# Optimization experiments

Hardware: AMD Instinct MI355X
Metric: run time of the kernel (lower is better)

The kernel has to match this reference:

```python
import jax, jax.numpy as jnp
import numpy as np

NH = 4        # router attention heads
M1, M2 = 16, 16  # Fourier modes kept
N_FNO_LAYERS = 4
TOP_K = 2
TEMP = 1.0


def _ln(x, g, b):
    m = x.mean(-1, keepdims=True)
    v = ((x - m) ** 2).mean(-1, keepdims=True)
    return (x - m) / jnp.sqrt(v + 1e-5) * g + b


def _mha(s, wqkv, bqkv, wo, bo):
    B, S, D = s.shape
    dh = D // NH
    qkv = s @ wqkv + bqkv
    q, k, v = jnp.split(qkv, 3, axis=-1)
    rs = lambda t: t.reshape(B, S, NH, dh).transpose(0, 2, 1, 3)
    q, k, v = rs(q), rs(k), rs(v)
    a = jax.nn.softmax(jnp.einsum('bhqd,bhkd->bhqk', q, k) / np.sqrt(dh), axis=-1)
    o = jnp.einsum('bhqk,bhkd->bhqd', a, v).transpose(0, 2, 1, 3).reshape(B, S, D)
    return o @ wo + bo


def _spectral_conv(h, w1, w2):
    # h: (B, Ci, H, W); w1/w2: (Ci, Co, M1, M2, 2) real/imag pairs
    B, Ci, H, W = h.shape
    Co = w1.shape[1]
    ft = jnp.fft.rfft2(h, axes=(-2, -1))  # (B, Ci, H, W//2+1) complex
    w1c = w1[..., 0] + 1j * w1[..., 1]
    w2c = w2[..., 0] + 1j * w2[..., 1]
    lo = jnp.einsum('bixy,ioxy->boxy', ft[:, :, :M1, :M2], w1c)
    hi = jnp.einsum('bixy,ioxy->boxy', ft[:, :, -M1:, :M2], w2c)
    oft = jnp.zeros((B, Co, H, W // 2 + 1), dtype=ft.dtype)
    oft = oft.at[:, :, :M1, :M2].set(lo).at[:, :, -M1:, :M2].set(hi)
    return jnp.fft.irfft2(oft, s=(H, W), axes=(-2, -1))


def _fno(x, lw, lb, sw1, sw2, kw, kb, p1w, p1b, p2w, p2b):
    h = jnp.einsum('bchw,co->bohw', x, lw) + lb[None, :, None, None]
    for l in range(N_FNO_LAYERS):
        s = _spectral_conv(h, sw1[l], sw2[l])
        sk = jnp.einsum('bchw,co->bohw', h, kw[l]) + kb[l][None, :, None, None]
        h = s + sk
        if l < N_FNO_LAYERS - 1:
            h = jax.nn.gelu(h)
    h = jax.nn.gelu(jnp.einsum('bchw,co->bohw', h, p1w) + p1b[None, :, None, None])
    return jnp.einsum('bchw,co->bohw', h, p2w) + p2b[None, :, None, None]


def _router(x, enc_in_w, enc_in_b, attn_wqkv, attn_bqkv, attn_wo, attn_bo,
            ln1_g, ln1_b, ffn_w1, ffn_b1, ffn_w2, ffn_b2, ln2_g, ln2_b, fc_w, fc_b):
    ic = x[:, :, 0, :]                       # (B, C, W) initial condition
    s = ic.transpose(0, 2, 1) @ enc_in_w + enc_in_b  # (B, W, hd)
    for l in range(attn_wqkv.shape[0]):
        s = _ln(s + _mha(s, attn_wqkv[l], attn_bqkv[l], attn_wo[l], attn_bo[l]), ln1_g[l], ln1_b[l])
        f = jax.nn.relu(s @ ffn_w1[l] + ffn_b1[l]) @ ffn_w2[l] + ffn_b2[l]
        s = _ln(s + f, ln2_g[l], ln2_b[l])
    feat = s.max(axis=1)                     # global max-pool over sequence
    logits = feat @ fc_w + fc_b              # (B, E)
    vals, idx = jax.lax.top_k(logits, TOP_K)
    w = jax.nn.softmax(vals / TEMP, axis=-1)
    B = logits.shape[0]
    rw = jnp.zeros_like(logits).at[jnp.arange(B)[:, None], idx].set(w)
    return rw


def setup_inputs() -> dict:
    key = jax.random.key(0)
    ks = iter(jax.random.split(key, 40))
    B, C, H, W = 32, 1, 64, 64
    E, HC, HD, RL, FF, OC = 8, 64, 64, 2, 256, 1
    rn = lambda shp, sc: jax.random.normal(next(ks), shp, dtype=jnp.float32) * sc
    inp = {
        'x': rn((B, C, H, W), 1.0),
        'enc_in_w': rn((C, HD), 0.5), 'enc_in_b': jnp.zeros((HD,), jnp.float32),
        'attn_wqkv': rn((RL, HD, 3 * HD), 0.08), 'attn_bqkv': jnp.zeros((RL, 3 * HD), jnp.float32),
        'attn_wo': rn((RL, HD, HD), 0.08), 'attn_bo': jnp.zeros((RL, HD), jnp.float32),
        'ln1_g': jnp.ones((RL, HD), jnp.float32), 'ln1_b': jnp.zeros((RL, HD), jnp.float32),
        'ffn_w1': rn((RL, HD, FF), 0.08), 'ffn_b1': jnp.zeros((RL, FF), jnp.float32),
        'ffn_w2': rn((RL, FF, HD), 0.05), 'ffn_b2': jnp.zeros((RL, HD), jnp.float32),
        'ln2_g': jnp.ones((RL, HD), jnp.float32), 'ln2_b': jnp.zeros((RL, HD), jnp.float32),
        'fc_w': rn((HD, E), 0.1), 'fc_b': jnp.zeros((E,), jnp.float32),
        'lift_w': rn((E, C, HC), 0.3), 'lift_b': jnp.zeros((E, HC), jnp.float32),
        'spec_w1': rn((E, N_FNO_LAYERS, HC, HC, M1, M2, 2), 1.0 / HC),
        'spec_w2': rn((E, N_FNO_LAYERS, HC, HC, M1, M2, 2), 1.0 / HC),
        'skip_w': rn((E, N_FNO_LAYERS, HC, HC), 0.08), 'skip_b': jnp.zeros((E, N_FNO_LAYERS, HC), jnp.float32),
        'proj1_w': rn((E, HC, HC), 0.08), 'proj1_b': jnp.zeros((E, HC), jnp.float32),
        'proj2_w': rn((E, HC, OC), 0.08), 'proj2_b': jnp.zeros((E, OC), jnp.float32),
    }
    return inp


def reference(x, enc_in_w, enc_in_b, attn_wqkv, attn_bqkv, attn_wo, attn_bo,
              ln1_g, ln1_b, ffn_w1, ffn_b1, ffn_w2, ffn_b2, ln2_g, ln2_b, fc_w, fc_b,
              lift_w, lift_b, spec_w1, spec_w2, skip_w, skip_b,
              proj1_w, proj1_b, proj2_w, proj2_b):
    rw = _router(x, enc_in_w, enc_in_b, attn_wqkv, attn_bqkv, attn_wo, attn_bo,
                 ln1_g, ln1_b, ffn_w1, ffn_b1, ffn_w2, ffn_b2, ln2_g, ln2_b, fc_w, fc_b)
    E = rw.shape[1]
    out = jnp.zeros((x.shape[0], proj2_w.shape[2], x.shape[2], x.shape[3]), x.dtype)
    for e in range(E):
        # weight is 0 for non-selected experts, so dense weighted sum == masked dispatch
        y = _fno(x, lift_w[e], lift_b[e], spec_w1[e], spec_w2[e],
                 skip_w[e], skip_b[e], proj1_w[e], proj1_b[e], proj2_w[e], proj2_b[e])
        out = out + rw[:, e, None, None, None] * y
    return out
```

## Files before the change

### kernel.cpp

```cpp
#include <hip/hip_runtime.h>
#include <math.h>

#define TWOPI_F 6.283185307179586f
#define LD4(p) (*(const float4*)(p))

__device__ __forceinline__ float gelu_f(float v) {
    float u = 0.7978845608028654f * (v + 0.044715f * v * v * v);
    return 0.5f * v * (1.f + tanhf(u));
}

__global__ void init_tables_kernel(float* __restrict__ Wy, float* __restrict__ TWX,
                                   float* __restrict__ WY2) {
    int t = threadIdx.x;
    for (int i = t; i < 1024; i += 256) {
        int y = i >> 4, k = i & 15;
        int m = (k * y) & 63;
        float a = -TWOPI_F * (float)m / 64.f;
        Wy[y * 32 + 2 * k]     = cosf(a);
        Wy[y * 32 + 2 * k + 1] = sinf(a);
    }
    for (int i = t; i < 2048; i += 256) {
        int x = i >> 5, kxm = i & 31;
        int kx = kxm < 16 ? kxm : kxm + 32;
        int m = (kx * x) & 63;
        float a = -TWOPI_F * (float)m / 64.f;
        TWX[x * 64 + 2 * kxm]     = cosf(a);
        TWX[x * 64 + 2 * kxm + 1] = sinf(a);
    }
    for (int i = t; i < 1024; i += 256) {
        int y = i >> 4, k = i & 15;
        int m = (k * y) & 63;
        float a = TWOPI_F * (float)m / 64.f;
        float sc = (k == 0 ? 1.f : 2.f) / 4096.f;
        WY2[y * 32 + 2 * k]     = sc * cosf(a);
        WY2[y * 32 + 2 * k + 1] = sc * sinf(a);
    }
}

__global__ __launch_bounds__(512) void router_kernel(
    const float* __restrict__ x, const float* __restrict__ enc_w, const float* __restrict__ enc_b,
    const float* __restrict__ wqkv, const float* __restrict__ bqkv,
    const float* __restrict__ wo, const float* __restrict__ bo,
    const float* __restrict__ ln1g, const float* __restrict__ ln1b,
    const float* __restrict__ w1, const float* __restrict__ b1,
    const float* __restrict__ w2, const float* __restrict__ b2,
    const float* __restrict__ ln2g, const float* __restrict__ ln2b,
    const float* __restrict__ fcw, const float* __restrict__ fcb,
    float* __restrict__ rw)
{
    __shared__ float s[64][65];
    __shared__ float qk[64][193];
    __shared__ float sc[64][65];
    __shared__ float o64[64][65];
    __shared__ float feat[64];
    __shared__ float logits[8];
    int b = blockIdx.x, t = threadIdx.x;

    for (int i = t; i < 4096; i += 512) {
        int w_ = i >> 6, d = i & 63;
        s[w_][d] = x[b * 4096 + w_] * enc_w[d] + enc_b[d];
    }
    __syncthreads();

    for (int l = 0; l < 2; ++l) {
        {
            const float* Wq = wqkv + l * 64 * 192;
            const float* Bq = bqkv + l * 192;
            int c4 = t % 48, rg = t / 48;
            if (rg < 8) {
                const float* wcol = Wq + 4 * c4;
                float4 bq = LD4(Bq + 4 * c4);
                float4 acc[8];
#pragma unroll
                for (int i = 0; i < 8; ++i) acc[i] = bq;
                int r0 = rg * 8;
#pragma unroll 8
                for (int k = 0; k < 64; ++k) {
                    float4 wv = LD4(wcol + k * 192);
#pragma unroll
                    for (int i = 0; i < 8; ++i) {
                        float sv = s[r0 + i][k];
                        acc[i].x += sv * wv.x; acc[i].y += sv * wv.y;
                        acc[i].z += sv * wv.z; acc[i].w += sv * wv.w;
                    }
                }
#pragma unroll
                for (int i = 0; i < 8; ++i) {
                    qk[r0 + i][4 * c4]     = acc[i].x;
                    qk[r0 + i][4 * c4 + 1] = acc[i].y;
                    qk[r0 + i][4 * c4 + 2] = acc[i].z;
                    qk[r0 + i][4 * c4 + 3] = acc[i].w;
                }
            }
        }
        __syncthreads();
        for (int h = 0; h < 4; ++h) {
            for (int i = t; i < 4096; i += 512) {
                int q = i >> 6, kj = i & 63;
                float acc = 0.f;
#pragma unroll
                for (int d = 0; d < 16; ++d)
                    acc += qk[q][h * 16 + d] * qk[kj][64 + h * 16 + d];
                sc[q][kj] = acc * 0.25f;
            }
            __syncthreads();
            if (t < 64) {
                float m = -1e30f;
                for (int j = 0; j < 64; ++j) m = fmaxf(m, sc[t][j]);
                float sum = 0.f;
                for (int j = 0; j < 64; ++j) { float e2 = expf(sc[t][j] - m); sc[t][j] = e2; sum += e2; }
                float inv = 1.f / sum;
                for (int j = 0; j < 64; ++j) sc[t][j] *= inv;
            }
            __syncthreads();
            for (int i = t; i < 1024; i += 512) {
                int q = i >> 4, d = i & 15;
                float acc = 0.f;
#pragma unroll 8
                for (int j = 0; j < 64; ++j) acc += sc[q][j] * qk[j][128 + h * 16 + d];
                o64[q][h * 16 + d] = acc;
            }
            __syncthreads();
        }
        {
            const float* Wo = wo + l * 4096;
            const float* Bo = bo + l * 64;
            int c4 = t & 15, rg = t >> 4;
            const float* wcol = Wo + 4 * c4;
            float4 acc0 = LD4(Bo + 4 * c4), acc1 = acc0;
            int r0 = rg * 2;
#pragma unroll 8
            for (int k = 0; k < 64; ++k) {
                float4 wv = LD4(wcol + k * 64);
                float h0 = o64[r0][k], h1 = o64[r0 + 1][k];
                acc0.x += h0 * wv.x; acc0.y += h0 * wv.y;
                acc0.z += h0 * wv.z; acc0.w += h0 * wv.w;
                acc1.x += h1 * wv.x; acc1.y += h1 * wv.y;
                acc1.z += h1 * wv.z; acc1.w += h1 * wv.w;
            }
            sc[r0][4 * c4]     = s[r0][4 * c4]     + acc0.x;
            sc[r0][4 * c4 + 1] = s[r0][4 * c4 + 1] + acc0.y;
            sc[r0][4 * c4 + 2] = s[r0][4 * c4 + 2] + acc0.z;
            sc[r0][4 * c4 + 3] = s[r0][4 * c4 + 3] + acc0.w;
            sc[r0 + 1][4 * c4]     = s[r0 + 1][4 * c4]     + acc1.x;
            sc[r0 + 1][4 * c4 + 1] = s[r0 + 1][4 * c4 + 1] + acc1.y;
            sc[r0 + 1][4 * c4 + 2] = s[r0 + 1][4 * c4 + 2] + acc1.z;
            sc[r0 + 1][4 * c4 + 3] = s[r0 + 1][4 * c4 + 3] + acc1.w;
        }
        __syncthreads();
        if (t < 64) {
            float m = 0.f;
            for (int j = 0; j < 64; ++j) m += sc[t][j];
            m *= (1.f / 64.f);
            float v = 0.f;
            for (int j = 0; j < 64; ++j) { float d = sc[t][j] - m; v += d * d; }
            v *= (1.f / 64.f);
            float inv = rsqrtf(v + 1e-5f);
            for (int j = 0; j < 64; ++j)
                s[t][j] = (sc[t][j] - m) * inv * ln1g[l * 64 + j] + ln1b[l * 64 + j];
        }
        __syncthreads();
        {
            const float* W1 = w1 + l * 64 * 256;
            const float* B1 = b1 + l * 256;
            int c4 = t & 63, rg = t >> 6;
            const float* wcol = W1 + 4 * c4;
            float4 b1v = LD4(B1 + 4 * c4);
            float4 acc[8];
#pragma unroll
            for (int i = 0; i < 8; ++i) acc[i] = b1v;
            int r0 = rg * 8;
#pragma unroll 4
            for (int k = 0; k < 64; ++k) {
                float4 wv = LD4(wcol + k * 256);
#pragma unroll
                for (int i = 0; i < 8; ++i) {
                    float sv = s[r0 + i][k];
                    acc[i].x += sv * wv.x; acc[i].y += sv * wv.y;
                    acc[i].z += sv * wv.z; acc[i].w += sv * wv.w;
                }
            }
#pragma unroll
            for (int i = 0; i < 8; ++i) {
                float a0 = fmaxf(acc[i].x, 0.f), a1 = fmaxf(acc[i].y, 0.f);
                float a2 = fmaxf(acc[i].z, 0.f), a3 = fmaxf(acc[i].w, 0.f);
                if (c4 < 48) {
                    qk[r0 + i][4 * c4] = a0; qk[r0 + i][4 * c4 + 1] = a1;
                    qk[r0 + i][4 * c4 + 2] = a2; qk[r0 + i][4 * c4 + 3] = a3;
                } else {
                    int c = 4 * c4 - 192;
                    o64[r0 + i][c] = a0; o64[r0 + i][c + 1] = a1;
                    o64[r0 + i][c + 2] = a2; o64[r0 + i][c + 3] = a3;
                }
            }
        }
        __syncthreads();
        {
            const float* W2 = w2 + l * 256 * 64;
            const float* B2 = b2 + l * 64;
            int c4 = t & 15, rg = t >> 4;
            const float* wcol = W2 + 4 * c4;
            float4 acc0 = LD4(B2 + 4 * c4), acc1 = acc0;
            int r0 = rg * 2;
#pragma unroll 8
            for (int k = 0; k < 192; ++k) {
                float4 wv = LD4(wcol + k * 64);
                float h0 = qk[r0][k], h1 = qk[r0 + 1][k];
                acc0.x += h0 * wv.x; acc0.y += h0 * wv.y;
                acc0.z += h0 * wv.z; acc0.w += h0 * wv.w;
                acc1.x += h1 * wv.x; acc1.y += h1 * wv.y;
                acc1.z += h1 * wv.z; acc1.w += h1 * wv.w;
            }
#pragma unroll 8
            for (int k = 192; k < 256; ++k) {
                float4 wv = LD4(wcol + k * 64);
                float h0 = o64[r0][k - 192], h1 = o64[r0 + 1][k - 192];
                acc0.x += h0 * wv.x; acc0.y += h0 * wv.y;
                acc0.z += h0 * wv.z; acc0.w += h0 * wv.w;
                acc1.x += h1 * wv.x; acc1.y += h1 * wv.y;
                acc1.z += h1 * wv.z; acc1.w += h1 * wv.w;
            }
            sc[r0][4 * c4]     = s[r0][4 * c4]     + acc0.x;
            sc[r0][4 * c4 + 1] = s[r0][4 * c4 + 1] + acc0.y;
            sc[r0][4 * c4 + 2] = s[r0][4 * c4 + 2] + acc0.z;
            sc[r0][4 * c4 + 3] = s[r0][4 * c4 + 3] + acc0.w;
            sc[r0 + 1][4 * c4]     = s[r0 + 1][4 * c4]     + acc1.x;
            sc[r0 + 1][4 * c4 + 1] = s[r0 + 1][4 * c4 + 1] + acc1.y;
            sc[r0 + 1][4 * c4 + 2] = s[r0 + 1][4 * c4 + 2] + acc1.z;
            sc[r0 + 1][4 * c4 + 3] = s[r0 + 1][4 * c4 + 3] + acc1.w;
        }
        __syncthreads();
        if (t < 64) {
            float m = 0.f;
            for (int j = 0; j < 64; ++j) m += sc[t][j];
            m *= (1.f / 64.f);
            float v = 0.f;
            for (int j = 0; j < 64; ++j) { float d = sc[t][j] - m; v += d * d; }
            v *= (1.f / 64.f);
            float inv = rsqrtf(v + 1e-5f);
            for (int j = 0; j < 64; ++j)
                s[t][j] = (sc[t][j] - m) * inv * ln2g[l * 64 + j] + ln2b[l * 64 + j];
        }
        __syncthreads();
    }
    if (t < 64) {
        float m = -1e30f;
        for (int r = 0; r < 64; ++r) m = fmaxf(m, s[r][t]);
        feat[t] = m;
    }
    __syncthreads();
    if (t < 8) {
        float acc = fcb[t];
        for (int k = 0; k < 64; ++k) acc += feat[k] * fcw[k * 8 + t];
        logits[t] = acc;
    }
    __syncthreads();
    if (t == 0) {
        int i0 = 0;
        for (int j = 1; j < 8; ++j) if (logits[j] > logits[i0]) i0 = j;
        int i1 = -1;
        for (int j = 0; j < 8; ++j) {
            if (j == i0) continue;
            if (i1 < 0 || logits[j] > logits[i1]) i1 = j;
        }
        float e1 = expf(logits[i1] - logits[i0]);
        float w0 = 1.f / (1.f + e1);
        float w1v = e1 / (1.f + e1);
        for (int j = 0; j < 8; ++j) rw[b * 8 + j] = 0.f;
        rw[b * 8 + i0] = w0;
        rw[b * 8 + i1] = w1v;
    }
}

__global__ void build_pairs_kernel(const float* __restrict__ rw, int* __restrict__ pair_b,
                                   int* __restrict__ pair_e, float* __restrict__ pair_w,
                                   int* __restrict__ estart, int* __restrict__ chunk_e,
                                   int* __restrict__ chunk_p0, int* __restrict__ chunk_np) {
    __shared__ float r[256];
    __shared__ int cnt[8], off[9];
    int t = threadIdx.x;
    for (int i = t; i < 256; i += 64) r[i] = rw[i];
    if (t < 64) { pair_b[t] = 0; pair_e[t] = 0; pair_w[t] = 0.f; }
    __syncthreads();
    if (t < 8) {
        int c = 0;
        for (int b = 0; b < 32; ++b) if (r[b * 8 + t] != 0.f) ++c;
        cnt[t] = c;
    }
    __syncthreads();
    if (t == 0) {
        int a = 0;
        for (int e = 0; e < 8; ++e) { off[e] = a; a += cnt[e]; }
        off[8] = a;
        for (int e = 0; e <= 8; ++e) estart[e] = off[e];
        int nc = 0;
        for (int e = 0; e < 8; ++e) {
            for (int s = off[e]; s < off[e + 1]; s += 8) {
                int np = off[e + 1] - s; if (np > 8) np = 8;
                chunk_e[nc] = e; chunk_p0[nc] = s; chunk_np[nc] = np; ++nc;
            }
        }
        for (int c = nc; c < 16; ++c) { chunk_e[c] = 0; chunk_p0[c] = 0; chunk_np[c] = 0; }
    }
    __syncthreads();
    if (t < 8) {
        int n = off[t];
        for (int b = 0; b < 32; ++b) {
            float w = r[b * 8 + t];
            if (w != 0.f) { pair_b[n] = b; pair_e[n] = t; pair_w[n] = w; ++n; }
        }
    }
}

__global__ __launch_bounds__(256) void lift_kernel(const float* __restrict__ x,
    const float* __restrict__ lw, const float* __restrict__ lb,
    const int* __restrict__ pair_b, const int* __restrict__ pair_e, float* __restrict__ hA) {
    int p = blockIdx.x, tile = blockIdx.y, t = threadIdx.x;
    int b = pair_b[p], e = pair_e[p];
    float* h = hA + (size_t)p * 262144;
    const float* xb = x + (size_t)b * 4096;
    for (int i = tile * 16384 + t; i < (tile + 1) * 16384; i += 256) {
        int co = i >> 12, xy = i & 4095;
        h[i] = xb[xy] * lw[e * 64 + co] + lb[e * 64 + co];
    }
}

__global__ __launch_bounds__(256) void fwdft_kernel(const float* __restrict__ h,
    const float* __restrict__ Wy, float* __restrict__ F) {
    __shared__ float ht[64][68];
    __shared__ float gt[64][36];
    __shared__ float wy[2048];
    __shared__ float tw64[128];
    int bid = blockIdx.x;
    int t = threadIdx.x;
    const float* src = h + (size_t)bid * 4096;
    for (int i = t; i < 1024; i += 256) {
        float4 v = *(const float4*)(src + i * 4);
        int x = (i * 4) >> 6, y = (i * 4) & 63;
        *(float4*)(&ht[x][y]) = v;
    }
    for (int i = t; i < 512; i += 256) *(float4*)(&wy[i * 4]) = *(const float4*)(Wy + i * 4);
    if (t < 64) {
        float a = -TWOPI_F * (float)t / 64.f;
        tw64[2 * t]     = cosf(a);
        tw64[2 * t + 1] = sinf(a);
    }
    __syncthreads();
    {
        int xx = t >> 2, kq = t & 3;
        float gr0 = 0.f, gi0 = 0.f, gr1 = 0.f, gi1 = 0.f;
        float gr2 = 0.f, gi2 = 0.f, gr3 = 0.f, gi3 = 0.f;
#pragma unroll 4
        for (int y = 0; y < 64; ++y) {
            float hv = ht[xx][y];
            float4 w0 = *(const float4*)(&wy[y * 32 + kq * 8]);
            float4 w1 = *(const float4*)(&wy[y * 32 + kq * 8 + 4]);
            gr0 += hv * w0.x; gi0 += hv * w0.y;
            gr1 += hv * w0.z; gi1 += hv * w0.w;
            gr2 += hv * w1.x; gi2 += hv * w1.y;
            gr3 += hv * w1.z; gi3 += hv * w1.w;
        }
        *(float4*)(&gt[xx][kq * 8])     = make_float4(gr0, gi0, gr1, gi1);
        *(float4*)(&gt[xx][kq * 8 + 4]) = make_float4(gr2, gi2, gr3, gi3);
    }
    __syncthreads();
    {
        int kxm = t & 31, kyq = t >> 5;
        int kx = kxm < 16 ? kxm : kxm + 32;
        float ar0 = 0.f, ai0 = 0.f, ar1 = 0.f, ai1 = 0.f;
        int idx = 0;
#pragma unroll 4
        for (int xx = 0; xx < 64; ++xx) {
            float c_ = tw64[2 * idx], s_ = tw64[2 * idx + 1];
            float4 g = *(const float4*)(&gt[xx][kyq * 4]);
            ar0 += g.x * c_ - g.y * s_;  ai0 += g.x * s_ + g.y * c_;
            ar1 += g.z * c_ - g.w * s_;  ai1 += g.z * s_ + g.w * c_;
            idx = (idx + kx) & 63;
        }
        float* fb = F + (size_t)bid * 1024 + kxm * 32 + kyq * 4;
        *(float4*)(fb) = make_float4(ar0, ai0, ar1, ai1);
    }
}

__global__ __launch_bounds__(256) void spectral_kernel(
    const float* __restrict__ F, float* __restrict__ FoA, float* __restrict__ FoB,
    const float* __restrict__ w1, const float* __restrict__ w2,
    const int* __restrict__ chunk_e, const int* __restrict__ chunk_p0,
    const int* __restrict__ chunk_np, int l)
{
    int c = blockIdx.x;
    int np = chunk_np[c];
    if (np == 0) return;
    int e = chunk_e[c], p0 = chunk_p0[c];
    int z = blockIdx.z;
    int wsel = z & 1, cih = (z >> 1) & 1, mq = z >> 2;
    int t = threadIdx.x;
    int co = blockIdx.y * 4 + (t >> 6);
    int lane = t & 63;
    int moff = mq * 256 + lane * 4;

    const float* wbase = (wsel == 0 ? w1 : w2) + (size_t)(e * 4 + l) * 2097152;
    const float* Wc  = wbase + (size_t)(cih * 32) * 32768 + (size_t)co * 512 + moff;
    const float* Fc0 = F + (size_t)p0 * 65536 + (size_t)(cih * 32) * 1024 + wsel * 512 + moff;
    float* Fob = (cih ? FoB : FoA) + (size_t)p0 * 65536 + (size_t)co * 1024 + wsel * 512 + moff;

    float4 acc[8];
#pragma unroll
    for (int p = 0; p < 8; ++p) acc[p] = make_float4(0.f, 0.f, 0.f, 0.f);
    const float* Wp = Wc;
    const float* Fp = Fc0;
    for (int ci = 0; ci < 32; ++ci) {
        float4 wv = LD4(Wp);
#pragma unroll
        for (int p = 0; p < 8; ++p) {
            float4 fv = LD4(Fp + (size_t)p * 65536);
            acc[p].x += fv.x * wv.x - fv.y * wv.y;
            acc[p].y += fv.x * wv.y + fv.y * wv.x;
            acc[p].z += fv.z * wv.z - fv.w * wv.w;
            acc[p].w += fv.z * wv.w + fv.w * wv.z;
        }
        Wp += 32768;
        Fp += 1024;
    }
#pragma unroll
    for (int p = 0; p < 8; ++p) {
        if (p < np)
            *(float4*)(Fob + (size_t)p * 65536) = acc[p];
    }
}

__global__ __launch_bounds__(256) void conv1x1_kernel(
    const float* __restrict__ src, float* __restrict__ dst,
    const float* __restrict__ Wall, const float* __restrict__ Ball,
    const int* __restrict__ pair_e, int wmul, int wadd, int do_gelu)
{
    __shared__ float ws[64][68];
    __shared__ float bs[64];
    int p = blockIdx.x, tile = blockIdx.y, t = threadIdx.x;
    int e = pair_e[p];
    int widx = e * wmul + wadd;
    const float* W = Wall + (size_t)widx * 4096;
    for (int i = t; i < 1024; i += 256) {
        float4 v = LD4(W + i * 4);
        int ci = (i * 4) >> 6, co = (i * 4) & 63;
        *(float4*)(&ws[ci][co]) = v;
    }
    if (t < 64) bs[t] = Ball[widx * 64 + t];
    __syncthreads();

    int xy4 = t & 63, cog = t >> 6;
    const float* sb = src + (size_t)p * 262144 + tile * 256 + xy4 * 4;
    float4 acc[16];
#pragma unroll
    for (int j = 0; j < 16; ++j) {
        float bv = bs[cog * 16 + j];
        acc[j] = make_float4(bv, bv, bv, bv);
    }
    for (int ci = 0; ci < 64; ++ci) {
        float4 sv = LD4(sb + (size_t)ci * 4096);
        float4 w0 = *(const float4*)(&ws[ci][cog * 16]);
        float4 w1 = *(const float4*)(&ws[ci][cog * 16 + 4]);
        float4 w2 = *(const float4*)(&ws[ci][cog * 16 + 8]);
        float4 w3 = *(const float4*)(&ws[ci][cog * 16 + 12]);
        float wr[16] = {w0.x, w0.y, w0.z, w0.w, w1.x, w1.y, w1.z, w1.w,
                        w2.x, w2.y, w2.z, w2.w, w3.x, w3.y, w3.z, w3.w};
#pragma unroll
        for (int j = 0; j < 16; ++j) {
            float w = wr[j];
            acc[j].x += sv.x * w; acc[j].y += sv.y * w;
            acc[j].z += sv.z * w; acc[j].w += sv.w * w;
        }
    }
    float* d = dst + (size_t)p * 262144 + (size_t)(cog * 16) * 4096 + tile * 256 + xy4 * 4;
#pragma unroll
    for (int j = 0; j < 16; ++j) {
        float4 v = acc[j];
        if (do_gelu) {
            v.x = gelu_f(v.x); v.y = gelu_f(v.y);
            v.z = gelu_f(v.z); v.w = gelu_f(v.w);
        }
        *(float4*)(d + (size_t)j * 4096) = v;
    }
}

__global__ __launch_bounds__(256) void inv_kernel(
    const float* __restrict__ FoA, const float* __restrict__ FoB,
    const float* __restrict__ WY2, float* __restrict__ dst_h, int do_gelu)
{
    __shared__ float wy2[2048];
    __shared__ float twl[128];
    __shared__ float fo_s[1024];
    __shared__ float tT[64][36];
    __shared__ float ot[64][66];
    int t = threadIdx.x;
    for (int i = t; i < 512; i += 256) *(float4*)(&wy2[i * 4]) = *(const float4*)(WY2 + i * 4);
    if (t < 64) {
        float a = TWOPI_F * (float)t / 64.f;
        twl[2 * t] = cosf(a);
        twl[2 * t + 1] = sinf(a);
    }
    __syncthreads();

    for (int item = 0; item < 4; ++item) {
        int wid = blockIdx.x * 4 + item;
        int p = wid >> 6, co = wid & 63;
        const float* fA = FoA + (size_t)p * 65536 + (size_t)co * 1024;
        const float* fB = FoB + (size_t)p * 65536 + (size_t)co * 1024;
        {
            float4 a = LD4(fA + t * 4);
            float4 b = LD4(fB + t * 4);
            *(float4*)(&fo_s[t * 4]) = make_float4(a.x + b.x, a.y + b.y, a.z + b.z, a.w + b.w);
        }
        __syncthreads();
        {
            int xx = t & 63, kq = t >> 6;
            float Tr0 = 0.f, Ti0 = 0.f, Tr1 = 0.f, Ti1 = 0.f;
            float Tr2 = 0.f, Ti2 = 0.f, Tr3 = 0.f, Ti3 = 0.f;
#pragma unroll 4
            for (int kxm = 0; kxm < 32; ++kxm) {
                int kx = kxm < 16 ? kxm : kxm + 32;
                int idx = (kx * xx) & 63;
                float c_ = twl[2 * idx], s_ = twl[2 * idx + 1];
                float4 f0 = *(const float4*)(&fo_s[kxm * 32 + kq * 8]);
                float4 f1 = *(const float4*)(&fo_s[kxm * 32 + kq * 8 + 4]);
                Tr0 += f0.x * c_ - f0.y * s_;  Ti0 += f0.x * s_ + f0.y * c_;
                Tr1 += f0.z * c_ - f0.w * s_;  Ti1 += f0.z * s_ + f0.w * c_;
                Tr2 += f1.x * c_ - f1.y * s_;  Ti2 += f1.x * s_ + f1.y * c_;
                Tr3 += f1.z * c_ - f1.w * s_;  Ti3 += f1.z * s_ + f1.w * c_;
            }
            *(float4*)(&tT[xx][kq * 8])     = make_float4(Tr0, Ti0, Tr1, Ti1);
            *(float4*)(&tT[xx][kq * 8 + 4]) = make_float4(Tr2, Ti2, Tr3, Ti3);
        }
        __syncthreads();
        {
            int xx = t & 63, yq = t >> 6;
            float Trr[16], Tii[16];
#pragma unroll
            for (int q = 0; q < 8; ++q) {
                float4 v = *(const float4*)(&tT[xx][q * 4]);
                Trr[q * 2] = v.x; Tii[q * 2] = v.y;
                Trr[q * 2 + 1] = v.z; Tii[q * 2 + 1] = v.w;
            }
            for (int j = 0; j < 16; ++j) {
                int y = yq * 16 + j;
                const float* wr = &wy2[y * 32];
                float acc = 0.f;
#pragma unroll
                for (int k = 0; k < 16; ++k)
                    acc += Trr[k] * wr[2 * k] - Tii[k] * wr[2 * k + 1];
                ot[xx][y] = acc;
            }
        }
        __syncthreads();
        {
            float* base = dst_h + (size_t)p * 262144 + (size_t)co * 4096;
            for (int r = 0; r < 16; ++r) {
                int gidx = r * 256 + t;
                int xx = gidx >> 6, y = gidx & 63;
                float v = base[gidx] + ot[xx][y];
                if (do_gelu) v = gelu_f(v);
                base[gidx] = v;
            }
        }
        __syncthreads();
    }
}

__global__ __launch_bounds__(256) void proj2_kernel(
    const float* __restrict__ hsrc, const float* __restrict__ p2w, const float* __restrict__ p2b,
    const int* __restrict__ pair_b, const int* __restrict__ pair_e,
    const float* __restrict__ pw, float* __restrict__ out)
{
    int p = blockIdx.x, tile = blockIdx.y, t = threadIdx.x;
    int b = pair_b[p], e = pair_e[p];
    float wgt = pw[p];
    const float* h = hsrc + (size_t)p * 262144 + tile * 256 + t;
    const float* w2 = p2w + e * 64;
    float acc = p2b[e];
#pragma unroll
    for (int c = 0; c < 64; ++c) acc += h[(size_t)c * 4096] * w2[c];
    atomicAdd(out + (size_t)b * 4096 + tile * 256 + t, wgt * acc);
}

extern "C" void kernel_launch(void* const* d_in, const int* in_sizes, int n_in,
                              void* d_out, int out_size, void* d_ws, size_t ws_size,
                              hipStream_t stream) {
    const float* x    = (const float*)d_in[0];
    const float* encw = (const float*)d_in[1];
    const float* encb = (const float*)d_in[2];
    const float* wqkv = (const float*)d_in[3];
    const float* bqkv = (const float*)d_in[4];
    const float* wo   = (const float*)d_in[5];
    const float* bo   = (const float*)d_in[6];
    const float* ln1g = (const float*)d_in[7];
    const float* ln1b = (const float*)d_in[8];
    const float* fw1  = (const float*)d_in[9];
    const float* fb1  = (const float*)d_in[10];
    const float* fw2  = (const float*)d_in[11];
    const float* fb2  = (const float*)d_in[12];
    const float* ln2g = (const float*)d_in[13];
    const float* ln2b = (const float*)d_in[14];
    const float* fcw  = (const float*)d_in[15];
    const float* fcb  = (const float*)d_in[16];
    const float* lw   = (const float*)d_in[17];
    const float* lb   = (const float*)d_in[18];
    const float* sw1  = (const float*)d_in[19];
    const float* sw2  = (const float*)d_in[20];
    const float* skw  = (const float*)d_in[21];
    const float* skb  = (const float*)d_in[22];
    const float* p1w  = (const float*)d_in[23];
    const float* p1b  = (const float*)d_in[24];
    const float* p2w  = (const float*)d_in[25];
    const float* p2b  = (const float*)d_in[26];
    float* out = (float*)d_out;

    float* wsf    = (float*)d_ws;
    float* rw     = wsf;
    float* pair_w = wsf + 256;
    int*   ipart  = (int*)(wsf + 320);
    int* pair_b   = ipart;
    int* pair_e   = ipart + 64;
    int* estart   = ipart + 128;
    int* chunk_e  = ipart + 137;
    int* chunk_p0 = ipart + 153;
    int* chunk_np = ipart + 169;
    float* Wy  = wsf + 512;
    float* TWX = wsf + 2560;
    float* WY2 = wsf + 6656;
    float* hA  = wsf + 16384;
    float* hB  = hA + (size_t)64 * 262144;
    float* F   = hB + (size_t)64 * 262144;
    float* FoA = F + (size_t)64 * 65536;
    float* FoB = FoA + (size_t)64 * 65536;
    size_t need = (16384 + 2ull * 64 * 262144 + 64ull * 65536 + 64ull * 131072) * 4;
    if (ws_size < need) return;

    hipMemsetAsync(d_out, 0, (size_t)out_size * sizeof(float), stream);
    init_tables_kernel<<<1, 256, 0, stream>>>(Wy, TWX, WY2);
    router_kernel<<<32, 512, 0, stream>>>(x, encw, encb, wqkv, bqkv, wo, bo, ln1g, ln1b,
                                          fw1, fb1, fw2, fb2, ln2g, ln2b, fcw, fcb, rw);
    build_pairs_kernel<<<1, 64, 0, stream>>>(rw, pair_b, pair_e, pair_w, estart,
                                             chunk_e, chunk_p0, chunk_np);
    lift_kernel<<<dim3(64, 16), 256, 0, stream>>>(x, lw, lb, pair_b, pair_e, hA);
    for (int l = 0; l < 4; ++l) {
        float* cur = (l & 1) ? hB : hA;
        float* nxt = (l & 1) ? hA : hB;
        fwdft_kernel<<<4096, 256, 0, stream>>>(cur, Wy, F);
        spectral_kernel<<<dim3(16, 16, 8), 256, 0, stream>>>(F, FoA, FoB, sw1, sw2,
                                                             chunk_e, chunk_p0, chunk_np, l);
        conv1x1_kernel<<<dim3(64, 16), 256, 0, stream>>>(cur, nxt, skw, skb, pair_e, 4, l, 0);
        inv_kernel<<<1024, 256, 0, stream>>>(FoA, FoB, WY2, nxt, (l < 3) ? 1 : 0);
    }
    conv1x1_kernel<<<dim3(64, 16), 256, 0, stream>>>(hA, hB, p1w, p1b, pair_e, 1, 0, 1);
    proj2_kernel<<<dim3(64, 16), 256, 0, stream>>>(hB, p2w, p2b, pair_b, pair_e, pair_w, out);
}
```

Baseline: 1.422 ms.

## Fuse projection layers, precompute twiddle tables, and split inverse DFT into more blocks

Merges the proj1 1x1 conv, GELU and the proj2 reduction into one kernel, so the full hidden tensor is no longer written to and re-read from global memory before the final projection. The per-block twiddle computation with cosf/sinf in the forward and inverse DFT kernels is replaced by a load of a small precomputed table. The inverse kernel now handles one (pair, channel) item per block across 4096 blocks instead of looping over 4 items per block, which gives more parallelism but repeats the WY2 table load per block.

Result: faster. 1.322 ms (-7.1%).

```diff
diff --git a/kernel.cpp b/kernel.cpp
--- a/kernel.cpp
+++ b/kernel.cpp
@@ -19,13 +19,12 @@
         Wy[y * 32 + 2 * k]     = cosf(a);
         Wy[y * 32 + 2 * k + 1] = sinf(a);
     }
-    for (int i = t; i < 2048; i += 256) {
-        int x = i >> 5, kxm = i & 31;
-        int kx = kxm < 16 ? kxm : kxm + 32;
-        int m = (kx * x) & 63;
-        float a = -TWOPI_F * (float)m / 64.f;
-        TWX[x * 64 + 2 * kxm]     = cosf(a);
-        TWX[x * 64 + 2 * kxm + 1] = sinf(a);
+    if (t < 64) {
+        float a = -TWOPI_F * (float)t / 64.f;
+        TWX[2 * t]           = cosf(a);
+        TWX[2 * t + 1]       = sinf(a);
+        TWX[128 + 2 * t]     = cosf(a);
+        TWX[128 + 2 * t + 1] = -sinf(a);
     }
     for (int i = t; i < 1024; i += 256) {
         int y = i >> 4, k = i & 15;
@@ -326,7 +325,7 @@
 }
 
 __global__ __launch_bounds__(256) void fwdft_kernel(const float* __restrict__ h,
-    const float* __restrict__ Wy, float* __restrict__ F) {
+    const float* __restrict__ Wy, const float* __restrict__ TWX, float* __restrict__ F) {
     __shared__ float ht[64][68];
     __shared__ float gt[64][36];
     __shared__ float wy[2048];
@@ -340,11 +339,7 @@
         *(float4*)(&ht[x][y]) = v;
     }
     for (int i = t; i < 512; i += 256) *(float4*)(&wy[i * 4]) = *(const float4*)(Wy + i * 4);
-    if (t < 64) {
-        float a = -TWOPI_F * (float)t / 64.f;
-        tw64[2 * t]     = cosf(a);
-        tw64[2 * t + 1] = sinf(a);
-    }
+    if (t < 32) *(float4*)(&tw64[t * 4]) = LD4(TWX + t * 4);
     __syncthreads();
     {
         int xx = t >> 2, kq = t & 3;
@@ -483,9 +478,79 @@
     }
 }
 
+__global__ __launch_bounds__(256) void projfused_kernel(
+    const float* __restrict__ src, const float* __restrict__ p1w,
+    const float* __restrict__ p1b, const float* __restrict__ p2w,
+    const float* __restrict__ p2b, const int* __restrict__ pair_b,
+    const int* __restrict__ pair_e, const float* __restrict__ pw,
+    float* __restrict__ out)
+{
+    __shared__ float ws[64][68];
+    __shared__ float bs[64];
+    __shared__ float w2s[64];
+    __shared__ float4 red[4][64];
+    int p = blockIdx.x, tile = blockIdx.y, t = threadIdx.x;
+    int e = pair_e[p];
+    const float* W = p1w + (size_t)e * 4096;
+    for (int i = t; i < 1024; i += 256) {
+        float4 v = LD4(W + i * 4);
+        int ci = (i * 4) >> 6, co = (i * 4) & 63;
+        *(float4*)(&ws[ci][co]) = v;
+    }
+    if (t < 64) { bs[t] = p1b[e * 64 + t]; w2s[t] = p2w[e * 64 + t]; }
+    __syncthreads();
+
+    int xy4 = t & 63, cog = t >> 6;
+    const float* sb = src + (size_t)p * 262144 + tile * 256 + xy4 * 4;
+    float4 acc[16];
+#pragma unroll
+    for (int j = 0; j < 16; ++j) {
+        float bv = bs[cog * 16 + j];
+        acc[j] = make_float4(bv, bv, bv, bv);
+    }
+    for (int ci = 0; ci < 64; ++ci) {
+        float4 sv = LD4(sb + (size_t)ci * 4096);
+        float4 w0 = *(const float4*)(&ws[ci][cog * 16]);
+        float4 w1 = *(const float4*)(&ws[ci][cog * 16 + 4]);
+        float4 w2 = *(const float4*)(&ws[ci][cog * 16 + 8]);
+        float4 w3 = *(const float4*)(&ws[ci][cog * 16 + 12]);
+        float wr[16] = {w0.x, w0.y, w0.z, w0.w, w1.x, w1.y, w1.z, w1.w,
+                        w2.x, w2.y, w2.z, w2.w, w3.x, w3.y, w3.z, w3.w};
+#pragma unroll
+        for (int j = 0; j < 16; ++j) {
+            float w = wr[j];
+            acc[j].x += sv.x * w; acc[j].y += sv.y * w;
+            acc[j].z += sv.z * w; acc[j].w += sv.w * w;
+        }
+    }
+    float4 part = make_float4(0.f, 0.f, 0.f, 0.f);
+#pragma unroll
+    for (int j = 0; j < 16; ++j) {
+        float w = w2s[cog * 16 + j];
+        part.x += gelu_f(acc[j].x) * w;
+        part.y += gelu_f(acc[j].y) * w;
+        part.z += gelu_f(acc[j].z) * w;
+        part.w += gelu_f(acc[j].w) * w;
+    }
+    red[cog][xy4] = part;
+    __syncthreads();
+    if (t < 64) {
+        float4 s0 = red[0][t], s1 = red[1][t], s2 = red[2][t], s3 = red[3][t];
+        float wgt = pw[p];
+        float b2 = p2b[e];
+        int b = pair_b[p];
+        float* ob = out + (size_t)b * 4096 + tile * 256 + t * 4;
+        atomicAdd(ob,     wgt * (s0.x + s1.x + s2.x + s3.x + b2));
+        atomicAdd(ob + 1, wgt * (s0.y + s1.y + s2.y + s3.y + b2));
+        atomicAdd(ob + 2, wgt * (s0.z + s1.z + s2.z + s3.z + b2));
+        atomicAdd(ob + 3, wgt * (s0.w + s1.w + s2.w + s3.w + b2));
+    }
+}
+
 __global__ __launch_bounds__(256) void inv_kernel(
     const float* __restrict__ FoA, const float* __restrict__ FoB,
-    const float* __restrict__ WY2, float* __restrict__ dst_h, int do_gelu)
+    const float* __restrict__ WY2, const float* __restrict__ TWX,
+    float* __restrict__ dst_h, int do_gelu)
 {
     __shared__ float wy2[2048];
     __shared__ float twl[128];
@@ -494,92 +559,67 @@
     __shared__ float ot[64][66];
     int t = threadIdx.x;
     for (int i = t; i < 512; i += 256) *(float4*)(&wy2[i * 4]) = *(const float4*)(WY2 + i * 4);
-    if (t < 64) {
-        float a = TWOPI_F * (float)t / 64.f;
-        twl[2 * t] = cosf(a);
-        twl[2 * t + 1] = sinf(a);
-    }
-    __syncthreads();
-
-    for (int item = 0; item < 4; ++item) {
-        int wid = blockIdx.x * 4 + item;
-        int p = wid >> 6, co = wid & 63;
-        const float* fA = FoA + (size_t)p * 65536 + (size_t)co * 1024;
-        const float* fB = FoB + (size_t)p * 65536 + (size_t)co * 1024;
-        {
-            float4 a = LD4(fA + t * 4);
-            float4 b = LD4(fB + t * 4);
-            *(float4*)(&fo_s[t * 4]) = make_float4(a.x + b.x, a.y + b.y, a.z + b.z, a.w + b.w);
-        }
-        __syncthreads();
-        {
-            int xx = t & 63, kq = t >> 6;
-            float Tr0 = 0.f, Ti0 = 0.f, Tr1 = 0.f, Ti1 = 0.f;
-            float Tr2 = 0.f, Ti2 = 0.f, Tr3 = 0.f, Ti3 = 0.f;
+    if (t < 32) *(float4*)(&twl[t * 4]) = LD4(TWX + 128 + t * 4);
+    int wid = blockIdx.x;
+    int p = wid >> 6, co = wid & 63;
+    const float* fA = FoA + (size_t)p * 65536 + (size_t)co * 1024;
+    const float* fB = FoB + (size_t)p * 65536 + (size_t)co * 1024;
+    {
+        float4 a = LD4(fA + t * 4);
+        float4 b = LD4(fB + t * 4);
+        *(float4*)(&fo_s[t * 4]) = make_float4(a.x + b.x, a.y + b.y, a.z + b.z, a.w + b.w);
+    }
+    __syncthreads();
+    {
+        int xx = t & 63, kq = t >> 6;
+        float Tr0 = 0.f, Ti0 = 0.f, Tr1 = 0.f, Ti1 = 0.f;
+        float Tr2 = 0.f, Ti2 = 0.f, Tr3 = 0.f, Ti3 = 0.f;
 #pragma unroll 4
-            for (int kxm = 0; kxm < 32; ++kxm) {
-                int kx = kxm < 16 ? kxm : kxm + 32;
-                int idx = (kx * xx) & 63;
-                float c_ = twl[2 * idx], s_ = twl[2 * idx + 1];
-                float4 f0 = *(const float4*)(&fo_s[kxm * 32 + kq * 8]);
-                float4 f1 = *(const float4*)(&fo_s[kxm * 32 + kq * 8 + 4]);
-                Tr0 += f0.x * c_ - f0.y * s_;  Ti0 += f0.x * s_ + f0.y * c_;
-                Tr1 += f0.z * c_ - f0.w * s_;  Ti1 += f0.z * s_ + f0.w * c_;
-                Tr2 += f1.x * c_ - f1.y * s_;  Ti2 += f1.x * s_ + f1.y * c_;
-                Tr3 += f1.z * c_ - f1.w * s_;  Ti3 += f1.z * s_ + f1.w * c_;
-            }
-            *(float4*)(&tT[xx][kq * 8])     = make_float4(Tr0, Ti0, Tr1, Ti1);
-            *(float4*)(&tT[xx][kq * 8 + 4]) = make_float4(Tr2, Ti2, Tr3, Ti3);
-        }
-        __syncthreads();
-        {
-            int xx = t & 63, yq = t >> 6;
-            float Trr[16], Tii[16];
-#pragma unroll
-            for (int q = 0; q < 8; ++q) {
-                float4 v = *(const float4*)(&tT[xx][q * 4]);
-                Trr[q * 2] = v.x; Tii[q * 2] = v.y;
-                Trr[q * 2 + 1] = v.z; Tii[q * 2 + 1] = v.w;
-            }
-            for (int j = 0; j < 16; ++j) {
-                int y = yq * 16 + j;
-                const float* wr = &wy2[y * 32];
-                float acc = 0.f;
-#pragma unroll
-                for (int k = 0; k < 16; ++k)
-                    acc += Trr[k] * wr[2 * k] - Tii[k] * wr[2 * k + 1];
-                ot[xx][y] = acc;
-            }
-        }
-        __syncthreads();
-        {
-            float* base = dst_h + (size_t)p * 262144 + (size_t)co * 4096;
-            for (int r = 0; r < 16; ++r) {
-                int gidx = r * 256 + t;
-                int xx = gidx >> 6, y = gidx & 63;
-                float v = base[gidx] + ot[xx][y];
-                if (do_gelu) v = gelu_f(v);
-                base[gidx] = v;
-            }
-        }
-        __syncthreads();
-    }
-}
-
-__global__ __launch_bounds__(256) void proj2_kernel(
-    const float* __restrict__ hsrc, const float* __restrict__ p2w, const float* __restrict__ p2b,
-    const int* __restrict__ pair_b, const int* __restrict__ pair_e,
-    const float* __restrict__ pw, float* __restrict__ out)
-{
-    int p = blockIdx.x, tile = blockIdx.y, t = threadIdx.x;
-    int b = pair_b[p], e = pair_e[p];
-    float wgt = pw[p];
-    const float* h = hsrc + (size_t)p * 262144 + tile * 256 + t;
-    const float* w2 = p2w + e * 64;
-    float acc = p2b[e];
-#pragma unroll
-    for (int c = 0; c < 64; ++c) acc += h[(size_t)c * 4096] * w2[c];
-    atomicAdd(out + (size_t)b * 4096 + tile * 256 + t, wgt * acc);
+        for (int kxm = 0; kxm < 32; ++kxm) {
+            int kx = kxm < 16 ? kxm : kxm + 32;
+            int idx = (kx * xx) & 63;
+            float c_ = twl[2 * idx], s_ = twl[2 * idx + 1];
+            float4 f0 = *(const float4*)(&fo_s[kxm * 32 + kq * 8]);
+            float4 f1 = *(const float4*)(&fo_s[kxm * 32 + kq * 8 + 4]);
+            Tr0 += f0.x * c_ - f0.y * s_;  Ti0 += f0.x * s_ + f0.y * c_;
+            Tr1 += f0.z * c_ - f0.w * s_;  Ti1 += f0.z * s_ + f0.w * c_;
+            Tr2 += f1.x * c_ - f1.y * s_;  Ti2 += f1.x * s_ + f1.y * c_;
+            Tr3 += f1.z * c_ - f1.w * s_;  Ti3 += f1.z * s_ + f1.w * c_;
+        }
+        *(float4*)(&tT[xx][kq * 8])     = make_float4(Tr0, Ti0, Tr1, Ti1);
+        *(float4*)(&tT[xx][kq * 8 + 4]) = make_float4(Tr2, Ti2, Tr3, Ti3);
+    }
+    __syncthreads();
+    {
+        int xx = t & 63, yq = t >> 6;
+        float Trr[16], Tii[16];
+#pragma unroll
+        for (int q = 0; q < 8; ++q) {
+            float4 v = *(const float4*)(&tT[xx][q * 4]);
+            Trr[q * 2] = v.x; Tii[q * 2] = v.y;
+            Trr[q * 2 + 1] = v.z; Tii[q * 2 + 1] = v.w;
+        }
+        for (int j = 0; j < 16; ++j) {
+            int y = yq * 16 + j;
+            const float* wr = &wy2[y * 32];
+            float acc = 0.f;
+#pragma unroll
+            for (int k = 0; k < 16; ++k)
+                acc += Trr[k] * wr[2 * k] - Tii[k] * wr[2 * k + 1];
+            ot[xx][y] = acc;
+        }
+    }
+    __syncthreads();
+    {
+        float* base = dst_h + (size_t)p * 262144 + (size_t)co * 4096;
+        for (int r = 0; r < 16; ++r) {
+            int gidx = r * 256 + t;
+            int xx = gidx >> 6, y = gidx & 63;
+            float v = base[gidx] + ot[xx][y];
+            if (do_gelu) v = gelu_f(v);
+            base[gidx] = v;
+        }
+    }
 }
 
 extern "C" void kernel_launch(void* const* d_in, const int* in_sizes, int n_in,
@@ -645,12 +685,12 @@
     for (int l = 0; l < 4; ++l) {
         float* cur = (l & 1) ? hB : hA;
         float* nxt = (l & 1) ? hA : hB;
-        fwdft_kernel<<<4096, 256, 0, stream>>>(cur, Wy, F);
+        fwdft_kernel<<<4096, 256, 0, stream>>>(cur, Wy, TWX, F);
         spectral_kernel<<<dim3(16, 16, 8), 256, 0, stream>>>(F, FoA, FoB, sw1, sw2,
                                                              chunk_e, chunk_p0, chunk_np, l);
         conv1x1_kernel<<<dim3(64, 16), 256, 0, stream>>>(cur, nxt, skw, skb, pair_e, 4, l, 0);
-        inv_kernel<<<1024, 256, 0, stream>>>(FoA, FoB, WY2, nxt, (l < 3) ? 1 : 0);
-    }
-    conv1x1_kernel<<<dim3(64, 16), 256, 0, stream>>>(hA, hB, p1w, p1b, pair_e, 1, 0, 1);
-    proj2_kernel<<<dim3(64, 16), 256, 0, stream>>>(hB, p2w, p2b, pair_b, pair_e, pair_w, out);
-}
+        inv_kernel<<<4096, 256, 0, stream>>>(FoA, FoB, WY2, TWX, nxt, (l < 3) ? 1 : 0);
+    }
+    projfused_kernel<<<dim3(64, 16), 256, 0, stream>>>(hA, p1w, p1b, p2w, p2b,
+                                                       pair_b, pair_e, pair_w, out);
+}
```
